# Optimization experiments

Measured on AMD Instinct MI355X. Metric: run time of the kernel, lower is better.

Reference implementation:

```python
import jax, jax.numpy as jnp
import numpy as np

D_MODEL = 1024
NUM_HEADS = 16
D_K = D_MODEL // NUM_HEADS
B, S = 4, 2048
NEG = -1e9


def setup_inputs() -> dict:
    key = jax.random.key(0)
    ks = jax.random.split(key, 12)
    def lin(kw, kb):
        bound = 1.0 / np.sqrt(D_MODEL)
        W = jax.random.uniform(kw, (D_MODEL, D_MODEL), jnp.float32, -bound, bound)
        b = jax.random.uniform(kb, (D_MODEL,), jnp.float32, -bound, bound)
        return W, b
    Wq, bq = lin(ks[0], ks[1])
    Wk, bk = lin(ks[2], ks[3])
    Wv, bv = lin(ks[4], ks[5])
    Wo, bo = lin(ks[6], ks[7])
    Q = jax.random.normal(ks[8], (B, S, D_MODEL), jnp.float32)
    K = jax.random.normal(ks[9], (B, S, D_MODEL), jnp.float32)
    V = jax.random.normal(ks[10], (B, S, D_MODEL), jnp.float32)
    # causal mask: 1 = keep, 0 = masked
    mask = jnp.tril(jnp.ones((S, S), jnp.int32))[None, None, :, :]
    mask = jnp.broadcast_to(mask, (B, 1, S, S))
    return {"Q": Q, "K": K, "V": V, "mask": mask,
            "Wq": Wq, "bq": bq, "Wk": Wk, "bk": bk,
            "Wv": Wv, "bv": bv, "Wo": Wo, "bo": bo}


def _split_heads(x):
    b, s, _ = x.shape
    return x.reshape(b, s, NUM_HEADS, D_K).transpose(0, 2, 1, 3)  # [B,H,S,Dk]


def reference(Q, K, V, mask, Wq, bq, Wk, bk, Wv, bv, Wo, bo):
    q = _split_heads(Q @ Wq.T + bq)
    k = _split_heads(K @ Wk.T + bk)
    v = _split_heads(V @ Wv.T + bv)
    scores = jnp.einsum('bhqd,bhkd->bhqk', q, k) / jnp.sqrt(jnp.float32(D_K))
    scores = jnp.where(mask == 0, jnp.float32(NEG), scores)
    probs = jax.nn.softmax(scores, axis=-1)
    attn = jnp.einsum('bhqk,bhkd->bhqd', probs, v)  # [B,H,S,Dk]
    attn = attn.transpose(0, 2, 1, 3).reshape(Q.shape[0], Q.shape[1], D_MODEL)
    return attn @ Wo.T + bo
```

## Files before the change

kernel.cpp:

```cpp
#include <hip/hip_runtime.h>
#include <hip/hip_bf16.h>
#include <cstdint>

typedef float floatx4 __attribute__((ext_vector_type(4)));
typedef __bf16 bf16x8 __attribute__((ext_vector_type(8)));

#define AS_G __attribute__((address_space(1)))
#define AS_L __attribute__((address_space(3)))

__device__ __forceinline__ void async_cp16(const void* g, void* l) {
    __builtin_amdgcn_global_load_lds((const AS_G uint32_t*)g, (AS_L uint32_t*)l, 16, 0, 0);
}

__device__ __forceinline__ floatx4 mfma16x16x32(bf16x8 a, bf16x8 b, floatx4 c) {
    return __builtin_amdgcn_mfma_f32_16x16x32_bf16(a, b, c, 0, 0, 0);
}

__device__ __forceinline__ unsigned short f2bf(float x) {
    return __builtin_bit_cast(unsigned short, (__bf16)x);
}

__global__ __launch_bounds__(256) void cvt_f32_bf16(const float* __restrict__ in,
                                                    unsigned short* __restrict__ out, int n) {
    int i = (blockIdx.x * 256 + threadIdx.x) * 4;
    if (i >= n) return;
    float4 v = *(const float4*)(in + i);
    ushort4 o;
    o.x = f2bf(v.x); o.y = f2bf(v.y); o.z = f2bf(v.z); o.w = f2bf(v.w);
    *(ushort4*)(out + i) = o;
}

__global__ __launch_bounds__(256) void cvt4_f32_bf16(const float* __restrict__ a, const float* __restrict__ b,
                                                     const float* __restrict__ c, const float* __restrict__ d,
                                                     unsigned short* __restrict__ out, int n) {
    const float* in = blockIdx.y == 0 ? a : blockIdx.y == 1 ? b : blockIdx.y == 2 ? c : d;
    unsigned short* o = out + (size_t)blockIdx.y * n;
    int i = (blockIdx.x * 256 + threadIdx.x) * 4;
    if (i >= n) return;
    float4 v = *(const float4*)(in + i);
    ushort4 u;
    u.x = f2bf(v.x); u.y = f2bf(v.y); u.z = f2bf(v.z); u.w = f2bf(v.w);
    *(ushort4*)(o + i) = u;
}

template <int MODE>
__global__ __launch_bounds__(256) void gemm_bt(const unsigned short* __restrict__ A,
                                               const unsigned short* __restrict__ W,
                                               const float* __restrict__ bias,
                                               float oscale,
                                               void* __restrict__ outv) {
    __shared__ unsigned short As[128 * 64];
    __shared__ unsigned short Bs[128 * 64];
    const int tid  = threadIdx.x;
    const int wave = tid >> 6, lane = tid & 63;
    const int quad = lane >> 4, l15 = lane & 15;
    const int l7   = l15 & 7;
    const int m0 = blockIdx.x * 128, n0 = blockIdx.y * 128;
    const int waveM = (wave >> 1) * 64, waveN = (wave & 1) * 64;

    floatx4 acc[4][4] = {};

    const int r8  = lane >> 3;
    const int gsw = (lane & 7) ^ r8;

    for (int k0 = 0; k0 < 1024; k0 += 64) {
        for (int c = wave; c < 16; c += 4) {
            const int row = c * 8 + r8;
            async_cp16(A + (size_t)(m0 + row) * 1024 + k0 + gsw * 8, (char*)As + c * 1024);
            async_cp16(W + (size_t)(n0 + row) * 1024 + k0 + gsw * 8, (char*)Bs + c * 1024);
        }
        __syncthreads();

#pragma unroll
        for (int h = 0; h < 2; ++h) {
            const int g = (quad + h * 4) ^ l7;
            bf16x8 af[4], bf[4];
#pragma unroll
            for (int t = 0; t < 4; ++t) {
                af[t] = *(const bf16x8*)&As[(waveM + t * 16 + l15) * 64 + g * 8];
                bf[t] = *(const bf16x8*)&Bs[(waveN + t * 16 + l15) * 64 + g * 8];
            }
#pragma unroll
            for (int mt = 0; mt < 4; ++mt)
#pragma unroll
                for (int nt = 0; nt < 4; ++nt)
                    acc[mt][nt] = mfma16x16x32(af[mt], bf[nt], acc[mt][nt]);
        }
        __syncthreads();
    }

#pragma unroll
    for (int mt = 0; mt < 4; ++mt) {
#pragma unroll
        for (int nt = 0; nt < 4; ++nt) {
            const int gcol = n0 + waveN + nt * 16 + l15;
            const float bv = bias[gcol];
#pragma unroll
            for (int r = 0; r < 4; ++r) {
                const int grow = m0 + waveM + mt * 16 + quad * 4 + r;
                const float val = (acc[mt][nt][r] + bv) * oscale;
                if (MODE == 2) {
                    ((float*)outv)[(size_t)grow * 1024 + gcol] = val;
                } else {
                    const int b = grow >> 11, s = grow & 2047;
                    const int h = gcol >> 6, dk = gcol & 63;
                    size_t idx;
                    if (MODE == 0) idx = ((size_t)(b * 16 + h) * 2048 + s) * 64 + dk;
                    else           idx = ((size_t)(b * 16 + h) * 64 + dk) * 2048 + s;
                    ((unsigned short*)outv)[idx] = f2bf(val);
                }
            }
        }
    }
}

#define PS_STRIDE 72

template <bool DIAG>
__device__ __forceinline__ void attn_tile(const unsigned short* __restrict__ Ks,
                                          const unsigned short* __restrict__ Vs,
                                          unsigned short* __restrict__ Psw,
                                          bf16x8 qf0, bf16x8 qf1,
                                          int quad, int l15,
                                          int qrow0,
                                          int kv0,
                                          float* __restrict__ lsum,
                                          floatx4* __restrict__ O) {
    const int l7 = l15 & 7;
    const int g1 = quad ^ l7, g2 = (quad + 4) ^ l7;

    floatx4 sc[4];
#pragma unroll
    for (int kvt = 0; kvt < 4; ++kvt) {
        const int rr = kvt * 16 + l15;
        floatx4 a = {};
        a = mfma16x16x32(qf0, *(const bf16x8*)&Ks[rr * 64 + g1 * 8], a);
        a = mfma16x16x32(qf1, *(const bf16x8*)&Ks[rr * 64 + g2 * 8], a);
        sc[kvt] = a;
    }

#pragma unroll
    for (int kvt = 0; kvt < 4; ++kvt) {
#pragma unroll
        for (int r = 0; r < 4; ++r) {
            float s = sc[kvt][r];
            if (DIAG && (kv0 + kvt * 16 + l15 > qrow0 + r)) s = -1.0e9f;
            const float p = __builtin_amdgcn_exp2f(s);
            lsum[r] += p;
            Psw[(quad * 4 + r) * PS_STRIDE + kvt * 16 + l15] = f2bf(p);
        }
    }

#pragma unroll
    for (int half = 0; half < 2; ++half) {
        bf16x8 pf = *(const bf16x8*)&Psw[l15 * PS_STRIDE + half * 32 + quad * 8];
        const int gb = (quad + half * 4) ^ l7;
#pragma unroll
        for (int nt = 0; nt < 4; ++nt) {
            bf16x8 vf = *(const bf16x8*)&Vs[(nt * 16 + l15) * 64 + gb * 8];
            O[nt] = mfma16x16x32(pf, vf, O[nt]);
        }
    }
}

__global__ __launch_bounds__(256) void flash_causal(const unsigned short* __restrict__ qp,
                                                    const unsigned short* __restrict__ kp,
                                                    const unsigned short* __restrict__ vt,
                                                    unsigned short* __restrict__ attn) {
    __shared__ unsigned short Ks[64 * 64];
    __shared__ unsigned short Vs[64 * 64];
    __shared__ unsigned short Ps[4 * 16 * PS_STRIDE];

    const int tid  = threadIdx.x;
    const int wave = tid >> 6, lane = tid & 63;
    const int quad = lane >> 4, l15 = lane & 15;
    const int bh = blockIdx.x;
    const int pr = blockIdx.y;
    const int tA = pr, tB = 31 - pr;

    unsigned short* Psw = &Ps[wave * 16 * PS_STRIDE];

    bf16x8 qfA0, qfA1, qfB0, qfB1;
    {
        const unsigned short* qa = qp + ((size_t)bh * 2048 + tA * 64 + wave * 16 + l15) * 64;
        qfA0 = *(const bf16x8*)(qa + quad * 8);
        qfA1 = *(const bf16x8*)(qa + 32 + quad * 8);
        const unsigned short* qb = qp + ((size_t)bh * 2048 + tB * 64 + wave * 16 + l15) * 64;
        qfB0 = *(const bf16x8*)(qb + quad * 8);
        qfB1 = *(const bf16x8*)(qb + 32 + quad * 8);
    }

    float lsumA[4] = {}, lsumB[4] = {};
    floatx4 OA[4] = {}, OB[4] = {};

    const int qrowA = tA * 64 + wave * 16 + quad * 4;
    const int qrowB = tB * 64 + wave * 16 + quad * 4;

    const int r8  = lane >> 3;
    const int gsw = (lane & 7) ^ r8;

    for (int t = 0; t <= tB; ++t) {
        const int kv0 = t * 64;
        for (int c = wave; c < 8; c += 4) {
            const int row = c * 8 + r8;
            async_cp16(kp + (size_t)bh * 131072 + (size_t)(kv0 + row) * 64 + gsw * 8,
                       (char*)Ks + c * 1024);
            async_cp16(vt + ((size_t)bh * 64 + row) * 2048 + kv0 + gsw * 8,
                       (char*)Vs + c * 1024);
        }
        __syncthreads();

        if (t == tB) attn_tile<true >(Ks, Vs, Psw, qfB0, qfB1, quad, l15, qrowB, kv0, lsumB, OB);
        else         attn_tile<false>(Ks, Vs, Psw, qfB0, qfB1, quad, l15, qrowB, kv0, lsumB, OB);
        if (t == tA)      attn_tile<true >(Ks, Vs, Psw, qfA0, qfA1, quad, l15, qrowA, kv0, lsumA, OA);
        else if (t < tA)  attn_tile<false>(Ks, Vs, Psw, qfA0, qfA1, quad, l15, qrowA, kv0, lsumA, OA);
        __syncthreads();
    }

    const int b = bh >> 4, h = bh & 15;
#pragma unroll
    for (int r = 0; r < 4; ++r) {
        float lA = lsumA[r], lB = lsumB[r];
#pragma unroll
        for (int off = 8; off; off >>= 1) {
            lA += __shfl_xor(lA, off, 16);
            lB += __shfl_xor(lB, off, 16);
        }
        const float invA = 1.0f / lA;
        const float invB = 1.0f / lB;
        const size_t rbA = ((size_t)b * 2048 + qrowA + r) * 1024 + h * 64;
        const size_t rbB = ((size_t)b * 2048 + qrowB + r) * 1024 + h * 64;
#pragma unroll
        for (int nt = 0; nt < 4; ++nt) {
            attn[rbA + nt * 16 + l15] = f2bf(OA[nt][r] * invA);
            attn[rbB + nt * 16 + l15] = f2bf(OB[nt][r] * invB);
        }
    }
}

extern "C" void kernel_launch(void* const* d_in, const int* in_sizes, int n_in,
                              void* d_out, int out_size, void* d_ws, size_t ws_size,
                              hipStream_t stream) {
    const float* Q  = (const float*)d_in[0];
    const float* K  = (const float*)d_in[1];
    const float* V  = (const float*)d_in[2];
    const float* Wq = (const float*)d_in[4];  const float* bq = (const float*)d_in[5];
    const float* Wk = (const float*)d_in[6];  const float* bk = (const float*)d_in[7];
    const float* Wv = (const float*)d_in[8];  const float* bv = (const float*)d_in[9];
    const float* Wo = (const float*)d_in[10]; const float* bo = (const float*)d_in[11];
    float* out = (float*)d_out;

    const int NIN = 8192 * 1024;
    const int NW  = 1024 * 1024;

    unsigned short* ws   = (unsigned short*)d_ws;
    unsigned short* inb  = ws;
    unsigned short* wb   = inb + NIN;
    unsigned short* qp   = wb + 4 * NW;
    unsigned short* kp   = qp + NIN;
    unsigned short* vtp  = kp + NIN;
    unsigned short* attnb = vtp + NIN;

    const float QSCL = 0.125f * 1.44269504088896f;

    dim3 blk(256);
    dim3 gcvtW((NW + 1023) / 1024, 4);
    dim3 gcvtA((NIN + 1023) / 1024);
    dim3 ggemm(64, 8);
    dim3 gflash(64, 16);

    cvt4_f32_bf16<<<gcvtW, blk, 0, stream>>>(Wq, Wk, Wv, Wo, wb, NW);

    cvt_f32_bf16<<<gcvtA, blk, 0, stream>>>(Q, inb, NIN);
    gemm_bt<0><<<ggemm, blk, 0, stream>>>(inb, wb + 0 * NW, bq, QSCL, (void*)qp);
    cvt_f32_bf16<<<gcvtA, blk, 0, stream>>>(K, inb, NIN);
    gemm_bt<0><<<ggemm, blk, 0, stream>>>(inb, wb + 1 * NW, bk, 1.0f, (void*)kp);
    cvt_f32_bf16<<<gcvtA, blk, 0, stream>>>(V, inb, NIN);
    gemm_bt<1><<<ggemm, blk, 0, stream>>>(inb, wb + 2 * NW, bv, 1.0f, (void*)vtp);

    flash_causal<<<gflash, blk, 0, stream>>>(qp, kp, vtp, attnb);

    gemm_bt<2><<<ggemm, blk, 0, stream>>>(attnb, wb + 3 * NW, bo, 1.0f, (void*)out);
}
```

Measured before the change: 363.6 us.

## Fuse input fp32-to-bf16 conversion into batched QKV projection GEMM

The three activation conversion kernels are removed. The Q/K/V projections are merged into one launch over blockIdx.z, and each block reads fp32 activations directly, converting them to bf16 into shared memory with register prefetch of the next k-tile. The output projection gets its own kernel with a smaller 64-row M tile, doubling the grid for better occupancy. This cuts the extra bf16 activation round-trip through memory and several launches, but loads A through registers instead of async LDS copies and reads twice the bytes per A element.

```diff
diff --git a/kernel.cpp b/kernel.cpp
--- a/kernel.cpp
+++ b/kernel.cpp
@@ -18,16 +18,6 @@
 
 __device__ __forceinline__ unsigned short f2bf(float x) {
     return __builtin_bit_cast(unsigned short, (__bf16)x);
-}
-
-__global__ __launch_bounds__(256) void cvt_f32_bf16(const float* __restrict__ in,
-                                                    unsigned short* __restrict__ out, int n) {
-    int i = (blockIdx.x * 256 + threadIdx.x) * 4;
-    if (i >= n) return;
-    float4 v = *(const float4*)(in + i);
-    ushort4 o;
-    o.x = f2bf(v.x); o.y = f2bf(v.y); o.z = f2bf(v.z); o.w = f2bf(v.w);
-    *(ushort4*)(out + i) = o;
 }
 
 __global__ __launch_bounds__(256) void cvt4_f32_bf16(const float* __restrict__ a, const float* __restrict__ b,
@@ -43,14 +33,22 @@
     *(ushort4*)(o + i) = u;
 }
 
-template <int MODE>
-__global__ __launch_bounds__(256) void gemm_bt(const unsigned short* __restrict__ A,
-                                               const unsigned short* __restrict__ W,
-                                               const float* __restrict__ bias,
-                                               float oscale,
-                                               void* __restrict__ outv) {
+__global__ __launch_bounds__(256) void gemm_proj(
+    const float* __restrict__ Qf, const float* __restrict__ Kf, const float* __restrict__ Vf,
+    const unsigned short* __restrict__ wball,
+    const float* __restrict__ bq, const float* __restrict__ bk, const float* __restrict__ bv,
+    float qscl,
+    unsigned short* __restrict__ qp, unsigned short* __restrict__ kp,
+    unsigned short* __restrict__ vtp) {
     __shared__ unsigned short As[128 * 64];
     __shared__ unsigned short Bs[128 * 64];
+    const int z = blockIdx.z;
+    const float* A = z == 0 ? Qf : z == 1 ? Kf : Vf;
+    const unsigned short* W = wball + (size_t)z * (1024 * 1024);
+    const float* bias = z == 0 ? bq : z == 1 ? bk : bv;
+    const float oscale = z == 0 ? qscl : 1.0f;
+    unsigned short* outp = z == 0 ? qp : z == 1 ? kp : vtp;
+
     const int tid  = threadIdx.x;
     const int wave = tid >> 6, lane = tid & 63;
     const int quad = lane >> 4, l15 = lane & 15;
@@ -61,15 +59,43 @@
     floatx4 acc[4][4] = {};
 
     const int r8  = lane >> 3;
-    const int gsw = (lane & 7) ^ r8;
+    const int gl  = lane & 7;
+    const int aphys = gl ^ r8;
+
+    const float* Abase = A + (size_t)(m0 + wave * 32 + r8) * 1024 + gl * 8;
+    float4 pa[4][2];
+#pragma unroll
+    for (int s = 0; s < 4; ++s) {
+        const float* p = Abase + (size_t)s * 8 * 1024;
+        pa[s][0] = *(const float4*)p;
+        pa[s][1] = *(const float4*)(p + 4);
+    }
 
     for (int k0 = 0; k0 < 1024; k0 += 64) {
         for (int c = wave; c < 16; c += 4) {
             const int row = c * 8 + r8;
-            async_cp16(A + (size_t)(m0 + row) * 1024 + k0 + gsw * 8, (char*)As + c * 1024);
-            async_cp16(W + (size_t)(n0 + row) * 1024 + k0 + gsw * 8, (char*)Bs + c * 1024);
-        }
-        __syncthreads();
+            async_cp16(W + (size_t)(n0 + row) * 1024 + k0 + (gl ^ r8) * 8, (char*)Bs + c * 1024);
+        }
+#pragma unroll
+        for (int s = 0; s < 4; ++s) {
+            const int row = wave * 32 + s * 8 + r8;
+            bf16x8 v;
+            v[0] = (__bf16)pa[s][0].x; v[1] = (__bf16)pa[s][0].y;
+            v[2] = (__bf16)pa[s][0].z; v[3] = (__bf16)pa[s][0].w;
+            v[4] = (__bf16)pa[s][1].x; v[5] = (__bf16)pa[s][1].y;
+            v[6] = (__bf16)pa[s][1].z; v[7] = (__bf16)pa[s][1].w;
+            *(bf16x8*)&As[row * 64 + aphys * 8] = v;
+        }
+        __syncthreads();
+
+        if (k0 + 64 < 1024) {
+#pragma unroll
+            for (int s = 0; s < 4; ++s) {
+                const float* p = Abase + (size_t)s * 8 * 1024 + (k0 + 64);
+                pa[s][0] = *(const float4*)p;
+                pa[s][1] = *(const float4*)(p + 4);
+            }
+        }
 
 #pragma unroll
         for (int h = 0; h < 2; ++h) {
@@ -94,21 +120,81 @@
 #pragma unroll
         for (int nt = 0; nt < 4; ++nt) {
             const int gcol = n0 + waveN + nt * 16 + l15;
-            const float bv = bias[gcol];
+            const float bv2 = bias[gcol];
 #pragma unroll
             for (int r = 0; r < 4; ++r) {
                 const int grow = m0 + waveM + mt * 16 + quad * 4 + r;
-                const float val = (acc[mt][nt][r] + bv) * oscale;
-                if (MODE == 2) {
-                    ((float*)outv)[(size_t)grow * 1024 + gcol] = val;
-                } else {
-                    const int b = grow >> 11, s = grow & 2047;
-                    const int h = gcol >> 6, dk = gcol & 63;
-                    size_t idx;
-                    if (MODE == 0) idx = ((size_t)(b * 16 + h) * 2048 + s) * 64 + dk;
-                    else           idx = ((size_t)(b * 16 + h) * 64 + dk) * 2048 + s;
-                    ((unsigned short*)outv)[idx] = f2bf(val);
-                }
+                const float val = (acc[mt][nt][r] + bv2) * oscale;
+                const int b = grow >> 11, s = grow & 2047;
+                const int h = gcol >> 6, dk = gcol & 63;
+                size_t idx;
+                if (z != 2) idx = ((size_t)(b * 16 + h) * 2048 + s) * 64 + dk;
+                else        idx = ((size_t)(b * 16 + h) * 64 + dk) * 2048 + s;
+                outp[idx] = f2bf(val);
+            }
+        }
+    }
+}
+
+__global__ __launch_bounds__(256) void gemm_out(const unsigned short* __restrict__ A,
+                                                const unsigned short* __restrict__ W,
+                                                const float* __restrict__ bias,
+                                                float* __restrict__ out) {
+    __shared__ unsigned short As[64 * 64];
+    __shared__ unsigned short Bs[128 * 64];
+    const int tid  = threadIdx.x;
+    const int wave = tid >> 6, lane = tid & 63;
+    const int quad = lane >> 4, l15 = lane & 15;
+    const int l7   = l15 & 15 & 7;
+    const int m0 = blockIdx.x * 64, n0 = blockIdx.y * 128;
+    const int waveM = (wave >> 1) * 32, waveN = (wave & 1) * 64;
+
+    floatx4 acc[2][4] = {};
+
+    const int r8  = lane >> 3;
+    const int gsw = (lane & 7) ^ r8;
+
+    for (int k0 = 0; k0 < 1024; k0 += 64) {
+        for (int c = wave; c < 24; c += 4) {
+            if (c < 8) {
+                const int row = c * 8 + r8;
+                async_cp16(A + (size_t)(m0 + row) * 1024 + k0 + gsw * 8, (char*)As + c * 1024);
+            } else {
+                const int row = (c - 8) * 8 + r8;
+                async_cp16(W + (size_t)(n0 + row) * 1024 + k0 + gsw * 8, (char*)Bs + (c - 8) * 1024);
+            }
+        }
+        __syncthreads();
+
+#pragma unroll
+        for (int h = 0; h < 2; ++h) {
+            const int g = (quad + h * 4) ^ l7;
+            bf16x8 af[2], bf[4];
+#pragma unroll
+            for (int t = 0; t < 2; ++t)
+                af[t] = *(const bf16x8*)&As[(waveM + t * 16 + l15) * 64 + g * 8];
+#pragma unroll
+            for (int t = 0; t < 4; ++t)
+                bf[t] = *(const bf16x8*)&Bs[(waveN + t * 16 + l15) * 64 + g * 8];
+#pragma unroll
+            for (int mt = 0; mt < 2; ++mt)
+#pragma unroll
+                for (int nt = 0; nt < 4; ++nt)
+                    acc[mt][nt] = mfma16x16x32(af[mt], bf[nt], acc[mt][nt]);
+        }
+        __syncthreads();
+    }
+
+#pragma unroll
+    for (int mt = 0; mt < 2; ++mt) {
+#pragma unroll
+        for (int nt = 0; nt < 4; ++nt) {
+            const int gcol = n0 + waveN + nt * 16 + l15;
+            const float bv = bias[gcol];
+#pragma unroll
+            for (int r = 0; r < 4; ++r) {
+                const int grow = m0 + waveM + mt * 16 + quad * 4 + r;
+                out[(size_t)grow * 1024 + gcol] = acc[mt][nt][r] + bv;
             }
         }
     }
@@ -254,8 +340,7 @@
     const int NW  = 1024 * 1024;
 
     unsigned short* ws   = (unsigned short*)d_ws;
-    unsigned short* inb  = ws;
-    unsigned short* wb   = inb + NIN;
+    unsigned short* wb   = ws;
     unsigned short* qp   = wb + 4 * NW;
     unsigned short* kp   = qp + NIN;
     unsigned short* vtp  = kp + NIN;
@@ -265,20 +350,15 @@
 
     dim3 blk(256);
     dim3 gcvtW((NW + 1023) / 1024, 4);
-    dim3 gcvtA((NIN + 1023) / 1024);
-    dim3 ggemm(64, 8);
+    dim3 gproj(64, 8, 3);
+    dim3 gout(128, 8);
     dim3 gflash(64, 16);
 
     cvt4_f32_bf16<<<gcvtW, blk, 0, stream>>>(Wq, Wk, Wv, Wo, wb, NW);
 
-    cvt_f32_bf16<<<gcvtA, blk, 0, stream>>>(Q, inb, NIN);
-    gemm_bt<0><<<ggemm, blk, 0, stream>>>(inb, wb + 0 * NW, bq, QSCL, (void*)qp);
-    cvt_f32_bf16<<<gcvtA, blk, 0, stream>>>(K, inb, NIN);
-    gemm_bt<0><<<ggemm, blk, 0, stream>>>(inb, wb + 1 * NW, bk, 1.0f, (void*)kp);
-    cvt_f32_bf16<<<gcvtA, blk, 0, stream>>>(V, inb, NIN);
-    gemm_bt<1><<<ggemm, blk, 0, stream>>>(inb, wb + 2 * NW, bv, 1.0f, (void*)vtp);
+    gemm_proj<<<gproj, blk, 0, stream>>>(Q, K, V, wb, bq, bk, bv, QSCL, qp, kp, vtp);
 
     flash_causal<<<gflash, blk, 0, stream>>>(qp, kp, vtp, attnb);
 
-    gemm_bt<2><<<ggemm, blk, 0, stream>>>(attnb, wb + 3 * NW, bo, 1.0f, (void*)out);
-}
+    gemm_out<<<gout, blk, 0, stream>>>(attnb, wb + 3 * NW, bo, out);
+}
```

Measured after the change: 378.5 us. +4.1%, slower.
